# Optimization experiments

Hardware: AMD Instinct MI355X
Metric: run time of the kernel (lower is better)

Reference implementation:

```python
import jax, jax.numpy as jnp
import numpy as np

APP_DIM = 27
FEA_PE = 6
VIEW_PE = 6
FEATURE_C = 128
DENSITY_SHIFT = -10.0
DISTANCE_SCALE = 25.0
IN_MLPC = 2 * VIEW_PE * 3 + 2 * FEA_PE * APP_DIM + 3 + APP_DIM  # 390


def positional_encoding(x, freqs):
    # x: [..., C] -> [..., 2*freqs*C]
    freq_bands = (2.0 ** jnp.arange(freqs)).astype(x.dtype)
    pts = (x[..., None] * freq_bands).reshape(x.shape[:-1] + (freqs * x.shape[-1],))
    return jnp.concatenate([jnp.sin(pts), jnp.cos(pts)], axis=-1)


def alpha2weights(alpha):
    # alpha: [N_rays, N_samples]; last sample forced opaque (as in source)
    alpha = alpha.at[:, -1].set(1.0)
    trans = jnp.concatenate(
        [jnp.ones((alpha.shape[0], 1), alpha.dtype), 1.0 - alpha + 1e-10], axis=-1)
    T = jnp.cumprod(trans, axis=-1)
    weights = alpha * T[:, :-1]
    return weights, T


def setup_inputs() -> dict:
    key = jax.random.key(0)
    ks = jax.random.split(key, 12)
    N_rays, N_samples = 4096, 128
    sigma_feat = jax.random.normal(ks[0], (N_rays, N_samples), jnp.float32)
    app_features = 0.1 * jax.random.normal(ks[1], (N_rays, N_samples, APP_DIM), jnp.float32)
    vd = jax.random.normal(ks[2], (N_rays, N_samples, 3), jnp.float32)
    viewdirs = vd / (jnp.linalg.norm(vd, axis=-1, keepdims=True) + 1e-8)
    dists = 0.02 * jax.random.uniform(ks[3], (N_rays, N_samples), jnp.float32)

    def linear(k, fan_in, fan_out):
        kw, kb = jax.random.split(k)
        lim = 1.0 / np.sqrt(fan_in)
        W = jax.random.uniform(kw, (fan_in, fan_out), jnp.float32, -lim, lim)
        b = jax.random.uniform(kb, (fan_out,), jnp.float32, -lim, lim)
        return W, b

    W1, b1 = linear(ks[4], IN_MLPC, FEATURE_C)
    W2, b2 = linear(ks[5], FEATURE_C, FEATURE_C)
    W3, _ = linear(ks[6], FEATURE_C, 3)
    b3 = jnp.zeros((3,), jnp.float32)  # bias of last layer initialized to 0 in source
    return {"sigma_feat": sigma_feat, "app_features": app_features,
            "viewdirs": viewdirs, "dists": dists,
            "W1": W1, "b1": b1, "W2": W2, "b2": b2, "W3": W3, "b3": b3}


def reference(sigma_feat, app_features, viewdirs, dists, W1, b1, W2, b2, W3, b3):
    # feature2density: softplus with density_shift
    sigma = jax.nn.softplus(sigma_feat + DENSITY_SHIFT)
    alpha = 1.0 - jnp.exp(-sigma * dists * DISTANCE_SCALE)  # [N_rays, N_samples]
    weights, _T = alpha2weights(alpha)

    # MLPRender_Fea: cat[features, viewdirs, PE(features), PE(viewdirs)]
    mlp_in = jnp.concatenate(
        [app_features, viewdirs,
         positional_encoding(app_features, FEA_PE),
         positional_encoding(viewdirs, VIEW_PE)], axis=-1)  # [R, S, 390]
    h = jax.nn.relu(jnp.einsum('rsc,cf->rsf', mlp_in, W1) + b1)
    h = jax.nn.relu(jnp.einsum('rsf,fg->rsg', h, W2) + b2)
    rgb = jax.nn.sigmoid(jnp.einsum('rsg,go->rso', h, W3) + b3)  # [R, S, 3]

    rgb_map = jnp.sum(weights[..., None] * rgb, axis=-2)  # [R, 3]
    return rgb_map
```

## Files before the change

### kernel.cpp

```cpp
#include <hip/hip_runtime.h>
#include <math.h>

typedef unsigned short u16;
using bf16x8 = __attribute__((ext_vector_type(8))) short;
using f32x4  = __attribute__((ext_vector_type(4))) float;

#define NS      128
#define RAYS_PER_BLOCK 2
#define NBLOCKS (4096 / RAYS_PER_BLOCK)
#define KS1     15
#define NSLICE  19

#define OW0   0
#define OW1   4096
#define OX0   8192
#define OX1   12288
#define OH1   8192
#define POOLSZ 24576

__device__ __forceinline__ u16 f2bf(float f) {
    unsigned int i = __float_as_uint(f);
    return (u16)((i + 0x7FFFu + ((i >> 16) & 1u)) >> 16);
}

__device__ __forceinline__ unsigned pk(float hi, float lo) {
    unsigned a = __float_as_uint(hi) + 0x8000u;
    unsigned b = __float_as_uint(lo) + 0x8000u;
    return __builtin_amdgcn_perm(a, b, 0x07060302u);
}
__device__ __forceinline__ u16 f2bf1(float f) {
    return (u16)((__float_as_uint(f) + 0x8000u) >> 16);
}

__device__ __forceinline__ int afoff(int m, int k) {
    return ((((k >> 5) * 8 + (m >> 4)) * 64) + (((k >> 3) & 3) * 16) + (m & 15)) * 8 + (k & 7);
}

__device__ __forceinline__ void stage_w(const u16* g, u16* l, int wave, int lane) {
    #pragma unroll
    for (int c = 0; c < 2; ++c) {
        const u16* gp = g + (wave * 2 + c) * 512 + lane * 8;
        u16* lp = l + (wave * 2 + c) * 512;
        __builtin_amdgcn_global_load_lds(
            (const __attribute__((address_space(1))) unsigned int*)gp,
            (__attribute__((address_space(3))) unsigned int*)lp, 16, 0, 0);
    }
}

__device__ __forceinline__ int orig_k(int ch, int slot) {
    if (ch < 27) {
        if (slot == 0) return ch;
        if (slot <= 6) return 30 + ch * 6 + (slot - 1);
        return 192 + ch * 6 + (slot - 7);
    } else {
        int c = ch - 27;
        if (slot == 0) return 27 + c;
        if (slot <= 6) return 354 + c * 6 + (slot - 1);
        return 372 + c * 6 + (slot - 7);
    }
}

__device__ __forceinline__ void build_x(u16* Xb, int m_b, int cl_b, float v) {
    float rev = v * 0.15915494309189535f;
    rev -= floorf(rev);
    float s0 = __builtin_amdgcn_sinf(rev);
    float c0 = __builtin_amdgcn_cosf(rev);
    float s1 = 2.f * s0 * c0, c1 = c0 * c0 - s0 * s0;
    float s2 = 2.f * s1 * c1, c2 = c1 * c1 - s1 * s1;
    float s3 = 2.f * s2 * c2, c3 = c2 * c2 - s2 * s2;
    float s4 = 2.f * s3 * c3, c4 = c3 * c3 - s3 * s3;
    float s5 = 2.f * s4 * c4, c5 = c4 * c4 - s4 * s4;
    uint4 lo, hi;
    lo.x = pk(s0, v);  lo.y = pk(s2, s1);  lo.z = pk(s4, s3);  lo.w = pk(c0, s5);
    hi.x = pk(c2, c1); hi.y = pk(c4, c3);  hi.z = pk(0.f, c5); hi.w = 0u;
    int base = (m_b >> 4) * 512 + ((2 * cl_b) * 16 + (m_b & 15)) * 8;
    *(uint4*)(Xb + base)       = lo;
    *(uint4*)(Xb + base + 128) = hi;
}

__global__ __launch_bounds__(256) void prep_kernel(
    const float* __restrict__ W1, const float* __restrict__ W2,
    const float* __restrict__ W3, u16* __restrict__ ws)
{
    int idx = blockIdx.x * 256 + threadIdx.x;
    if (idx < 61440) {
        int j = idx & 7, lane = (idx >> 3) & 63, nt = (idx >> 9) & 7, ks = idx >> 12;
        int q = lane >> 4, l15 = lane & 15;
        int klocal = q * 8 + j;
        int ch = ks * 2 + (klocal >> 4);
        int slot = klocal & 15;
        int n = nt * 16 + l15;
        ws[idx] = (slot < 13) ? f2bf(W1[orig_k(ch, slot) * 128 + n]) : (u16)0;
    } else if (idx < 77824) {
        int i2 = idx - 61440;
        int j = i2 & 7, lane = (i2 >> 3) & 63, nt = (i2 >> 9) & 7, ks = i2 >> 12;
        int k = ks * 32 + (lane >> 4) * 8 + j;
        int n = nt * 16 + (lane & 15);
        ws[idx] = f2bf(W2[k * 128 + n]);
    } else if (idx < 79872) {
        int i3 = idx - 77824;
        int j = i3 & 7, lane = (i3 >> 3) & 63, ks = i3 >> 9;
        int k = ks * 32 + (lane >> 4) * 8 + j;
        int n = lane & 15;
        ws[idx] = (n < 3) ? f2bf(W3[k * 3 + n]) : (u16)0;
    }
}

__global__ __launch_bounds__(256, 3) void render_kernel(
    const float* __restrict__ sigma_g, const float* __restrict__ app_g,
    const float* __restrict__ view_g,  const float* __restrict__ dists_g,
    const float* __restrict__ b1_g,    const float* __restrict__ b2_g,
    const float* __restrict__ b3_g,    const u16* __restrict__ ws,
    float* __restrict__ out_g)
{
    __shared__ __align__(16) u16 pool[POOLSZ];
    __shared__ float scanS;
    __shared__ float sum2[6];
    float* part = (float*)(pool + OW0);

    const int tid  = threadIdx.x;
    const int lane = tid & 63;
    const int wave = tid >> 6;
    const int l15  = lane & 15;
    const int quad = lane >> 4;
    const int wm   = wave >> 1;
    const int wn   = wave & 1;

    const u16* w3r = ws + 77824;

    float b1r[4], b2r[4];
    #pragma unroll
    for (int nt = 0; nt < 4; ++nt) {
        int col = wn * 64 + nt * 16 + l15;
        b1r[nt] = b1_g[col];
        b2r[nt] = b2_g[col];
    }
    const float b3v = (l15 < 3) ? b3_g[l15] : 0.f;
    bf16x8 w3fr[4];
    #pragma unroll
    for (int ks = 0; ks < 4; ++ks)
        w3fr[ks] = *(const bf16x8*)(w3r + (ks * 64 + lane) * 8);

    const int m_b  = tid >> 1;
    const int cl_b = tid & 1;

    #pragma unroll 1
    for (int ri = 0; ri < RAYS_PER_BLOCK; ++ri) {
        const int r  = blockIdx.x * RAYS_PER_BLOCK + ri;
        const int rb = r * NS;
        const float* ap = app_g  + (rb + m_b) * 27;
        const float* vp = view_g + (rb + m_b) * 3;

        float pv_cur = ap[cl_b];
        float pv_nxt = ap[2 + cl_b];

        stage_w(ws, pool + OW0, wave, lane);

        float alpha = 0.f, prod = 1.f, wr = 0.f;
        if (tid < NS) {
            float x  = sigma_g[rb + tid] - 10.f;
            float sp = (x > 20.f) ? x : log1pf(expf(x));
            alpha = 1.f - expf(-sp * dists_g[rb + tid] * 25.f);
            if (tid == NS - 1) alpha = 1.f;
            float tb = 1.f - alpha + 1e-10f;
            prod = tb;
            #pragma unroll
            for (int d = 1; d < 64; d <<= 1) {
                float v = __shfl_up(prod, d);
                if (lane >= d) prod *= v;
            }
            if (tid == 63) scanS = prod;
        }

        build_x(pool + OX0, m_b, cl_b, pv_cur);
        pv_cur = pv_nxt;
        __syncthreads();

        if (tid < NS) {
            float prev = __shfl_up(prod, 1);
            float base = (lane == 0) ? 1.f : prev;
            float scale = (wave == 1) ? scanS : 1.f;
            wr = alpha * base * scale;
        }

        const f32x4 vzero = {0.f, 0.f, 0.f, 0.f};
        f32x4 acc[4][4];
        #pragma unroll
        for (int mt = 0; mt < 4; ++mt)
            #pragma unroll
            for (int nt = 0; nt < 4; ++nt) acc[mt][nt] = vzero;

        #pragma unroll 1
        for (int i = 0; i < NSLICE; ++i) {
            if (i + 1 < NSLICE)
                stage_w(ws + (i + 1) * 4096,
                        pool + ((((i + 1) & 1) == 0) ? OW0 : OW1), wave, lane);
            if (i + 2 < KS1) {
                int ch = 2 * (i + 2) + cl_b;
                pv_nxt = (ch < 27) ? ap[ch] : vp[ch - 27];
            }

            const u16* Wb = pool + (((i & 1) == 0) ? OW0 : OW1);
            const u16* Asrc = (i < KS1)
                ? (pool + (((i & 1) == 0) ? OX0 : OX1))
                : (pool + OH1 + (i - KS1) * 4096);
            bf16x8 a[4];
            #pragma unroll
            for (int mt = 0; mt < 4; ++mt)
                a[mt] = *(const bf16x8*)(Asrc + ((wm * 4 + mt) * 64 + lane) * 8);
            #pragma unroll
            for (int nt = 0; nt < 4; ++nt) {
                bf16x8 b = *(const bf16x8*)(Wb + ((wn * 4 + nt) * 64 + lane) * 8);
                #pragma unroll
                for (int mt = 0; mt < 4; ++mt)
                    acc[mt][nt] = __builtin_amdgcn_mfma_f32_16x16x32_bf16(a[mt], b, acc[mt][nt], 0, 0, 0);
            }
            if (i < KS1 - 1) {
                u16* Xb = pool + ((((i + 1) & 1) == 0) ? OX0 : OX1);
                build_x(Xb, m_b, cl_b, pv_cur);
                pv_cur = pv_nxt;
            }
            if (i == KS1 - 1) {
                __syncthreads();
                #pragma unroll
                for (int mt = 0; mt < 4; ++mt)
                    #pragma unroll
                    for (int nt = 0; nt < 4; ++nt) {
                        int col = wn * 64 + nt * 16 + l15;
                        #pragma unroll
                        for (int rr = 0; rr < 4; ++rr) {
                            int row = wm * 64 + mt * 16 + quad * 4 + rr;
                            pool[OH1 + afoff(row, col)] =
                                f2bf1(fmaxf(acc[mt][nt][rr] + b1r[nt], 0.f));
                        }
                        acc[mt][nt] = vzero;
                    }
            }
            __syncthreads();
        }

        #pragma unroll
        for (int mt = 0; mt < 4; ++mt)
            #pragma unroll
            for (int nt = 0; nt < 4; ++nt) {
                int col = wn * 64 + nt * 16 + l15;
                #pragma unroll
                for (int rr = 0; rr < 4; ++rr) {
                    int row = wm * 64 + mt * 16 + quad * 4 + rr;
                    pool[OH1 + afoff(row, col)] =
                        f2bf1(fmaxf(acc[mt][nt][rr] + b2r[nt], 0.f));
                }
            }
        __syncthreads();

        f32x4 acc3[2] = {vzero, vzero};
        #pragma unroll
        for (int mi = 0; mi < 2; ++mi) {
            int mtt = wn * 2 + mi;
            #pragma unroll
            for (int ks = 0; ks < 4; ++ks) {
                bf16x8 a3 = *(const bf16x8*)(pool + OH1 + ks * 4096 +
                    ((wm * 4 + mtt) * 64 + lane) * 8);
                acc3[mi] = __builtin_amdgcn_mfma_f32_16x16x32_bf16(a3, w3fr[ks], acc3[mi], 0, 0, 0);
            }
        }
        if (l15 < 3) {
            #pragma unroll
            for (int mi = 0; mi < 2; ++mi) {
                int mtt = wn * 2 + mi;
                #pragma unroll
                for (int rr = 0; rr < 4; ++rr) {
                    int row = wm * 64 + mtt * 16 + quad * 4 + rr;
                    float v = acc3[mi][rr] + b3v;
                    part[row * 3 + l15] = 1.f / (1.f + expf(-v));
                }
            }
        }
        __syncthreads();

        float v0 = 0.f, v1 = 0.f, v2 = 0.f;
        if (tid < NS) {
            v0 = wr * part[tid * 3 + 0];
            v1 = wr * part[tid * 3 + 1];
            v2 = wr * part[tid * 3 + 2];
            #pragma unroll
            for (int d = 1; d < 64; d <<= 1) {
                v0 += __shfl_xor(v0, d);
                v1 += __shfl_xor(v1, d);
                v2 += __shfl_xor(v2, d);
            }
            if (lane == 0) {
                sum2[wave * 3 + 0] = v0;
                sum2[wave * 3 + 1] = v1;
                sum2[wave * 3 + 2] = v2;
            }
        }
        __syncthreads();
        if (tid == 0) {
            out_g[r * 3 + 0] = sum2[0] + sum2[3];
            out_g[r * 3 + 1] = sum2[1] + sum2[4];
            out_g[r * 3 + 2] = sum2[2] + sum2[5];
        }
        __syncthreads();
    }
}

extern "C" void kernel_launch(void* const* d_in, const int* in_sizes, int n_in,
                              void* d_out, int out_size, void* d_ws, size_t ws_size,
                              hipStream_t stream) {
    (void)in_sizes; (void)n_in; (void)out_size; (void)ws_size;
    const float* sigma = (const float*)d_in[0];
    const float* app   = (const float*)d_in[1];
    const float* view  = (const float*)d_in[2];
    const float* dists = (const float*)d_in[3];
    const float* W1    = (const float*)d_in[4];
    const float* b1    = (const float*)d_in[5];
    const float* W2    = (const float*)d_in[6];
    const float* b2    = (const float*)d_in[7];
    const float* W3    = (const float*)d_in[8];
    const float* b3    = (const float*)d_in[9];
    float* out = (float*)d_out;

    u16* ws = (u16*)d_ws;

    prep_kernel<<<312, 256, 0, stream>>>(W1, W2, W3, ws);
    render_kernel<<<NBLOCKS, 256, 0, stream>>>(sigma, app, view, dists,
                                               b1, b2, b3, ws, out);
}
```

Before: 218.0 us.

## Use 512-thread blocks per ray with weights loaded from global to registers

Each block now handles one ray with 8 waves (2x4 wave grid) instead of two rays sequentially with 4 waves. Weight fragments are now read straight from global memory into registers and double-buffered there, rather than staged through LDS with global_load_lds. The hidden-activation LDS layout gets an XOR swizzle to cut bank conflicts. The bf16 pack helper now uses the hardware cvt_pk_bf16 instruction. Together these shrink LDS use and raise per-block parallelism. The cost is more global/L2 traffic for weights and half the threads sitting idle during input building.

```diff
diff --git a/kernel.cpp b/kernel.cpp
--- a/kernel.cpp
+++ b/kernel.cpp
@@ -6,17 +6,13 @@
 using f32x4  = __attribute__((ext_vector_type(4))) float;
 
 #define NS      128
-#define RAYS_PER_BLOCK 2
-#define NBLOCKS (4096 / RAYS_PER_BLOCK)
+#define NBLOCKS 4096
 #define KS1     15
 #define NSLICE  19
 
-#define OW0   0
-#define OW1   4096
-#define OX0   8192
-#define OX1   12288
-#define OH1   8192
-#define POOLSZ 24576
+#define OX0   0
+#define OX1   4096
+#define POOLSZ 16384
 
 __device__ __forceinline__ u16 f2bf(float f) {
     unsigned int i = __float_as_uint(f);
@@ -24,27 +20,18 @@
 }
 
 __device__ __forceinline__ unsigned pk(float hi, float lo) {
-    unsigned a = __float_as_uint(hi) + 0x8000u;
-    unsigned b = __float_as_uint(lo) + 0x8000u;
-    return __builtin_amdgcn_perm(a, b, 0x07060302u);
+    unsigned r;
+    asm("v_cvt_pk_bf16_f32 %0, %1, %2" : "=v"(r) : "v"(lo), "v"(hi));
+    return r;
 }
 __device__ __forceinline__ u16 f2bf1(float f) {
     return (u16)((__float_as_uint(f) + 0x8000u) >> 16);
 }
 
-__device__ __forceinline__ int afoff(int m, int k) {
-    return ((((k >> 5) * 8 + (m >> 4)) * 64) + (((k >> 3) & 3) * 16) + (m & 15)) * 8 + (k & 7);
-}
-
-__device__ __forceinline__ void stage_w(const u16* g, u16* l, int wave, int lane) {
-    #pragma unroll
-    for (int c = 0; c < 2; ++c) {
-        const u16* gp = g + (wave * 2 + c) * 512 + lane * 8;
-        u16* lp = l + (wave * 2 + c) * 512;
-        __builtin_amdgcn_global_load_lds(
-            (const __attribute__((address_space(1))) unsigned int*)gp,
-            (__attribute__((address_space(3))) unsigned int*)lp, 16, 0, 0);
-    }
+__device__ __forceinline__ int afoff_h(int m, int k) {
+    int chunk = ((k >> 5) * 8 + (m >> 4)) * 64 + ((k >> 3) & 3) * 16 + (m & 15);
+    chunk ^= (k >> 3) & 3;
+    return chunk * 8 + (k & 7);
 }
 
 __device__ __forceinline__ int orig_k(int ch, int slot) {
@@ -106,7 +93,7 @@
     }
 }
 
-__global__ __launch_bounds__(256, 3) void render_kernel(
+__global__ __launch_bounds__(512, 4) void render_kernel(
     const float* __restrict__ sigma_g, const float* __restrict__ app_g,
     const float* __restrict__ view_g,  const float* __restrict__ dists_g,
     const float* __restrict__ b1_g,    const float* __restrict__ b2_g,
@@ -114,24 +101,24 @@
     float* __restrict__ out_g)
 {
     __shared__ __align__(16) u16 pool[POOLSZ];
+    __shared__ __align__(16) float part[NS * 3];
     __shared__ float scanS;
     __shared__ float sum2[6];
-    float* part = (float*)(pool + OW0);
 
     const int tid  = threadIdx.x;
     const int lane = tid & 63;
     const int wave = tid >> 6;
     const int l15  = lane & 15;
     const int quad = lane >> 4;
-    const int wm   = wave >> 1;
-    const int wn   = wave & 1;
+    const int wm   = wave >> 2;
+    const int wn   = wave & 3;
 
     const u16* w3r = ws + 77824;
 
-    float b1r[4], b2r[4];
-    #pragma unroll
-    for (int nt = 0; nt < 4; ++nt) {
-        int col = wn * 64 + nt * 16 + l15;
+    float b1r[2], b2r[2];
+    #pragma unroll
+    for (int nt = 0; nt < 2; ++nt) {
+        int col = wn * 32 + nt * 16 + l15;
         b1r[nt] = b1_g[col];
         b2r[nt] = b2_g[col];
     }
@@ -141,167 +128,173 @@
     for (int ks = 0; ks < 4; ++ks)
         w3fr[ks] = *(const bf16x8*)(w3r + (ks * 64 + lane) * 8);
 
-    const int m_b  = tid >> 1;
-    const int cl_b = tid & 1;
-
-    #pragma unroll 1
-    for (int ri = 0; ri < RAYS_PER_BLOCK; ++ri) {
-        const int r  = blockIdx.x * RAYS_PER_BLOCK + ri;
-        const int rb = r * NS;
-        const float* ap = app_g  + (rb + m_b) * 27;
-        const float* vp = view_g + (rb + m_b) * 3;
-
-        float pv_cur = ap[cl_b];
-        float pv_nxt = ap[2 + cl_b];
-
-        stage_w(ws, pool + OW0, wave, lane);
-
-        float alpha = 0.f, prod = 1.f, wr = 0.f;
-        if (tid < NS) {
-            float x  = sigma_g[rb + tid] - 10.f;
-            float sp = (x > 20.f) ? x : log1pf(expf(x));
-            alpha = 1.f - expf(-sp * dists_g[rb + tid] * 25.f);
-            if (tid == NS - 1) alpha = 1.f;
-            float tb = 1.f - alpha + 1e-10f;
-            prod = tb;
-            #pragma unroll
-            for (int d = 1; d < 64; d <<= 1) {
-                float v = __shfl_up(prod, d);
-                if (lane >= d) prod *= v;
-            }
-            if (tid == 63) scanS = prod;
-        }
-
+    const int r  = blockIdx.x;
+    const int rb = r * NS;
+    const int  m_b     = (tid >> 1) & 127;
+    const int  cl_b    = tid & 1;
+    const bool builder = (tid < 256);
+    const float* ap = app_g  + (rb + m_b) * 27;
+    const float* vp = view_g + (rb + m_b) * 3;
+
+    float pv_cur = 0.f, pv_nxt = 0.f;
+    if (builder) {
+        pv_cur = ap[cl_b];
+        pv_nxt = ap[2 + cl_b];
+    }
+
+    float alpha = 0.f, prod = 1.f, wr = 0.f;
+    if (tid < NS) {
+        float x  = sigma_g[rb + tid] - 10.f;
+        float sp = (x > 20.f) ? x : log1pf(expf(x));
+        alpha = 1.f - expf(-sp * dists_g[rb + tid] * 25.f);
+        if (tid == NS - 1) alpha = 1.f;
+        float tb = 1.f - alpha + 1e-10f;
+        prod = tb;
+        #pragma unroll
+        for (int d = 1; d < 64; d <<= 1) {
+            float v = __shfl_up(prod, d);
+            if (lane >= d) prod *= v;
+        }
+        if (tid == 63) scanS = prod;
+    }
+
+    if (builder) {
         build_x(pool + OX0, m_b, cl_b, pv_cur);
         pv_cur = pv_nxt;
-        __syncthreads();
-
-        if (tid < NS) {
-            float prev = __shfl_up(prod, 1);
-            float base = (lane == 0) ? 1.f : prev;
-            float scale = (wave == 1) ? scanS : 1.f;
-            wr = alpha * base * scale;
-        }
-
-        const f32x4 vzero = {0.f, 0.f, 0.f, 0.f};
-        f32x4 acc[4][4];
-        #pragma unroll
-        for (int mt = 0; mt < 4; ++mt)
-            #pragma unroll
-            for (int nt = 0; nt < 4; ++nt) acc[mt][nt] = vzero;
-
-        #pragma unroll 1
-        for (int i = 0; i < NSLICE; ++i) {
-            if (i + 1 < NSLICE)
-                stage_w(ws + (i + 1) * 4096,
-                        pool + ((((i + 1) & 1) == 0) ? OW0 : OW1), wave, lane);
-            if (i + 2 < KS1) {
-                int ch = 2 * (i + 2) + cl_b;
-                pv_nxt = (ch < 27) ? ap[ch] : vp[ch - 27];
-            }
-
-            const u16* Wb = pool + (((i & 1) == 0) ? OW0 : OW1);
-            const u16* Asrc = (i < KS1)
-                ? (pool + (((i & 1) == 0) ? OX0 : OX1))
-                : (pool + OH1 + (i - KS1) * 4096);
-            bf16x8 a[4];
+    }
+    __syncthreads();
+
+    if (tid < NS) {
+        float prev = __shfl_up(prod, 1);
+        float base = (lane == 0) ? 1.f : prev;
+        float scale = (wave == 1) ? scanS : 1.f;
+        wr = alpha * base * scale;
+    }
+
+    const f32x4 vzero = {0.f, 0.f, 0.f, 0.f};
+    f32x4 acc[4][2];
+    #pragma unroll
+    for (int mt = 0; mt < 4; ++mt)
+        #pragma unroll
+        for (int nt = 0; nt < 2; ++nt) acc[mt][nt] = vzero;
+
+    const u16* wp0 = ws + (wn * 128 + lane) * 8;
+    bf16x8 bA[2], bB[2];
+    bA[0] = *(const bf16x8*)(wp0);
+    bA[1] = *(const bf16x8*)(wp0 + 512);
+
+    auto body = [&](int i, bf16x8* bc, bf16x8* bn) {
+        if (i + 1 < NSLICE) {
+            const u16* wp = wp0 + (i + 1) * 4096;
+            bn[0] = *(const bf16x8*)(wp);
+            bn[1] = *(const bf16x8*)(wp + 512);
+        }
+        if (builder && i + 2 < KS1) {
+            int ch = 2 * (i + 2) + cl_b;
+            pv_nxt = (ch < 27) ? ap[ch] : vp[ch - 27];
+        }
+        bf16x8 a[4];
+        if (i < KS1) {
+            const u16* Asrc = pool + (((i & 1) == 0) ? OX0 : OX1);
             #pragma unroll
             for (int mt = 0; mt < 4; ++mt)
                 a[mt] = *(const bf16x8*)(Asrc + ((wm * 4 + mt) * 64 + lane) * 8);
-            #pragma unroll
-            for (int nt = 0; nt < 4; ++nt) {
-                bf16x8 b = *(const bf16x8*)(Wb + ((wn * 4 + nt) * 64 + lane) * 8);
+        } else {
+            #pragma unroll
+            for (int mt = 0; mt < 4; ++mt) {
+                int c = (i - KS1) * 512 + (wm * 4 + mt) * 64 + lane;
+                a[mt] = *(const bf16x8*)(pool + (c ^ quad) * 8);
+            }
+        }
+        #pragma unroll
+        for (int nt = 0; nt < 2; ++nt)
+            #pragma unroll
+            for (int mt = 0; mt < 4; ++mt)
+                acc[mt][nt] = __builtin_amdgcn_mfma_f32_16x16x32_bf16(
+                    a[mt], bc[nt], acc[mt][nt], 0, 0, 0);
+        if (builder && i < KS1 - 1) {
+            u16* Xb = pool + ((((i + 1) & 1) == 0) ? OX0 : OX1);
+            build_x(Xb, m_b, cl_b, pv_cur);
+            pv_cur = pv_nxt;
+        }
+        if (i == KS1 - 1) {
+            __syncthreads();
+            #pragma unroll
+            for (int mt = 0; mt < 4; ++mt)
                 #pragma unroll
-                for (int mt = 0; mt < 4; ++mt)
-                    acc[mt][nt] = __builtin_amdgcn_mfma_f32_16x16x32_bf16(a[mt], b, acc[mt][nt], 0, 0, 0);
+                for (int nt = 0; nt < 2; ++nt) {
+                    int col = wn * 32 + nt * 16 + l15;
+                    #pragma unroll
+                    for (int rr = 0; rr < 4; ++rr) {
+                        int row = wm * 64 + mt * 16 + quad * 4 + rr;
+                        pool[afoff_h(row, col)] =
+                            f2bf1(fmaxf(acc[mt][nt][rr] + b1r[nt], 0.f));
+                    }
+                    acc[mt][nt] = vzero;
+                }
+        }
+        __syncthreads();
+    };
+
+    #pragma unroll 1
+    for (int t = 0; t < 9; ++t) {
+        body(2 * t,     bA, bB);
+        body(2 * t + 1, bB, bA);
+    }
+    body(18, bA, bB);
+
+    #pragma unroll
+    for (int mt = 0; mt < 4; ++mt)
+        #pragma unroll
+        for (int nt = 0; nt < 2; ++nt) {
+            int col = wn * 32 + nt * 16 + l15;
+            #pragma unroll
+            for (int rr = 0; rr < 4; ++rr) {
+                int row = wm * 64 + mt * 16 + quad * 4 + rr;
+                pool[afoff_h(row, col)] =
+                    f2bf1(fmaxf(acc[mt][nt][rr] + b2r[nt], 0.f));
             }
-            if (i < KS1 - 1) {
-                u16* Xb = pool + ((((i + 1) & 1) == 0) ? OX0 : OX1);
-                build_x(Xb, m_b, cl_b, pv_cur);
-                pv_cur = pv_nxt;
-            }
-            if (i == KS1 - 1) {
-                __syncthreads();
-                #pragma unroll
-                for (int mt = 0; mt < 4; ++mt)
-                    #pragma unroll
-                    for (int nt = 0; nt < 4; ++nt) {
-                        int col = wn * 64 + nt * 16 + l15;
-                        #pragma unroll
-                        for (int rr = 0; rr < 4; ++rr) {
-                            int row = wm * 64 + mt * 16 + quad * 4 + rr;
-                            pool[OH1 + afoff(row, col)] =
-                                f2bf1(fmaxf(acc[mt][nt][rr] + b1r[nt], 0.f));
-                        }
-                        acc[mt][nt] = vzero;
-                    }
-            }
-            __syncthreads();
-        }
-
-        #pragma unroll
-        for (int mt = 0; mt < 4; ++mt)
-            #pragma unroll
-            for (int nt = 0; nt < 4; ++nt) {
-                int col = wn * 64 + nt * 16 + l15;
-                #pragma unroll
-                for (int rr = 0; rr < 4; ++rr) {
-                    int row = wm * 64 + mt * 16 + quad * 4 + rr;
-                    pool[OH1 + afoff(row, col)] =
-                        f2bf1(fmaxf(acc[mt][nt][rr] + b2r[nt], 0.f));
-                }
-            }
-        __syncthreads();
-
-        f32x4 acc3[2] = {vzero, vzero};
-        #pragma unroll
-        for (int mi = 0; mi < 2; ++mi) {
-            int mtt = wn * 2 + mi;
-            #pragma unroll
-            for (int ks = 0; ks < 4; ++ks) {
-                bf16x8 a3 = *(const bf16x8*)(pool + OH1 + ks * 4096 +
-                    ((wm * 4 + mtt) * 64 + lane) * 8);
-                acc3[mi] = __builtin_amdgcn_mfma_f32_16x16x32_bf16(a3, w3fr[ks], acc3[mi], 0, 0, 0);
-            }
-        }
-        if (l15 < 3) {
-            #pragma unroll
-            for (int mi = 0; mi < 2; ++mi) {
-                int mtt = wn * 2 + mi;
-                #pragma unroll
-                for (int rr = 0; rr < 4; ++rr) {
-                    int row = wm * 64 + mtt * 16 + quad * 4 + rr;
-                    float v = acc3[mi][rr] + b3v;
-                    part[row * 3 + l15] = 1.f / (1.f + expf(-v));
-                }
-            }
-        }
-        __syncthreads();
-
-        float v0 = 0.f, v1 = 0.f, v2 = 0.f;
-        if (tid < NS) {
-            v0 = wr * part[tid * 3 + 0];
-            v1 = wr * part[tid * 3 + 1];
-            v2 = wr * part[tid * 3 + 2];
-            #pragma unroll
-            for (int d = 1; d < 64; d <<= 1) {
-                v0 += __shfl_xor(v0, d);
-                v1 += __shfl_xor(v1, d);
-                v2 += __shfl_xor(v2, d);
-            }
-            if (lane == 0) {
-                sum2[wave * 3 + 0] = v0;
-                sum2[wave * 3 + 1] = v1;
-                sum2[wave * 3 + 2] = v2;
-            }
-        }
-        __syncthreads();
-        if (tid == 0) {
-            out_g[r * 3 + 0] = sum2[0] + sum2[3];
-            out_g[r * 3 + 1] = sum2[1] + sum2[4];
-            out_g[r * 3 + 2] = sum2[2] + sum2[5];
-        }
-        __syncthreads();
+        }
+    __syncthreads();
+
+    f32x4 acc3 = vzero;
+    #pragma unroll
+    for (int ks = 0; ks < 4; ++ks) {
+        int c = (ks * 8 + wave) * 64 + lane;
+        bf16x8 a3 = *(const bf16x8*)(pool + (c ^ quad) * 8);
+        acc3 = __builtin_amdgcn_mfma_f32_16x16x32_bf16(a3, w3fr[ks], acc3, 0, 0, 0);
+    }
+    if (l15 < 3) {
+        #pragma unroll
+        for (int rr = 0; rr < 4; ++rr) {
+            int row = wave * 16 + quad * 4 + rr;
+            float v = acc3[rr] + b3v;
+            part[row * 3 + l15] = 1.f / (1.f + expf(-v));
+        }
+    }
+    __syncthreads();
+
+    if (tid < NS) {
+        float v0 = wr * part[tid * 3 + 0];
+        float v1 = wr * part[tid * 3 + 1];
+        float v2 = wr * part[tid * 3 + 2];
+        #pragma unroll
+        for (int d = 1; d < 64; d <<= 1) {
+            v0 += __shfl_xor(v0, d);
+            v1 += __shfl_xor(v1, d);
+            v2 += __shfl_xor(v2, d);
+        }
+        if (lane == 0) {
+            sum2[wave * 3 + 0] = v0;
+            sum2[wave * 3 + 1] = v1;
+            sum2[wave * 3 + 2] = v2;
+        }
+    }
+    __syncthreads();
+    if (tid == 0) {
+        out_g[r * 3 + 0] = sum2[0] + sum2[3];
+        out_g[r * 3 + 1] = sum2[1] + sum2[4];
+        out_g[r * 3 + 2] = sum2[2] + sum2[5];
     }
 }
 
@@ -324,6 +317,6 @@
     u16* ws = (u16*)d_ws;
 
     prep_kernel<<<312, 256, 0, stream>>>(W1, W2, W3, ws);
-    render_kernel<<<NBLOCKS, 256, 0, stream>>>(sigma, app, view, dists,
+    render_kernel<<<NBLOCKS, 512, 0, stream>>>(sigma, app, view, dists,
                                                b1, b2, b3, ws, out);
 }
```

Result: slower. 254.4 us (+16.7%).
